# Kernel tuning notes

Hardware: AMD Instinct MI355X
Metric: run time of the kernel (lower is better)

## Reference

```python
import jax, jax.numpy as jnp
import numpy as np

B, H, W = 64, 512, 512
HW = H * W
MIN_, MAX_ = 100, 100          # seeds sampled per image (bg, fg)
MIN_P, MAX_P = 0.3, 0.3        # candidate-pool fractions
FG_ERODE_K, FG_ERODE_ITER = 11, 1
KSZ = 3                        # dilation kernel for seed maps
IGNORE_IDX = -255
N_BG = int(MIN_P * H * W)      # static bottom-n pool size
EPS = 1e-8


def _minpool2d(x, k):  # morphological erosion of binary map (geodesic border)
    return jax.lax.reduce_window(x, np.inf, jax.lax.min, (k, k), (1, 1), 'SAME')


def _maxpool3d(x, k):  # morphological dilation over (b,h,w)
    return jax.lax.reduce_window(x, -np.inf, jax.lax.max, (1, k, k), (1, 1, 1), 'SAME')


def _gumbel(u):
    return -jnp.log(-jnp.log(u))


def _one_sample(cam, u_fg, u_bg, th):
    # cam: [H,W] in [0,1]; u_fg/u_bg: [HW] uniform(0,1); th: scalar threshold
    cam_q = jnp.floor(cam * 255.0)
    th = jnp.where(th == 0.0, 1.0, jnp.where(th == 255.0, 254.0, th))
    deg = cam.min() == cam.max()  # degenerate map -> no seeds
    roi = (cam_q > th).astype(jnp.float32)
    for _ in range(FG_ERODE_ITER):
        roi = _minpool2d(roi, FG_ERODE_K)

    # ---- foreground: top-n of cam*roi, weighted sample max_ w/o replacement
    camr = (cam * roi + EPS).reshape(HW)
    n_fg = jnp.floor(MAX_P * roi.sum()).astype(jnp.int32)
    order = jnp.argsort(-camr, stable=True)                 # descending stable
    rank = jnp.zeros(HW, jnp.int32).at[order].set(jnp.arange(HW, dtype=jnp.int32))
    mask = rank < n_fg
    logp = jnp.log(jnp.where(mask, camr, 1.0))              # weighted: p = cam value
    score = jnp.where(mask, logp + _gumbel(u_fg), -jnp.inf) # Gumbel top-k == multinomial w/o repl.
    _, sel = jax.lax.top_k(score, MAX_)
    valid = (jnp.arange(MAX_) < jnp.minimum(MAX_, n_fg)) & (n_fg > 0) & (~deg)
    fg = jnp.zeros(HW, jnp.int32).at[sel].set(valid.astype(jnp.int32))

    # ---- background: bottom-n of cam, weighted by relu(1-cam)+eps
    camb = (cam + EPS).reshape(HW)
    orderb = jnp.argsort(camb, stable=True)                 # ascending stable
    rankb = jnp.zeros(HW, jnp.int32).at[orderb].set(jnp.arange(HW, dtype=jnp.int32))
    maskb = rankb < N_BG
    pb = jax.nn.relu(1.0 - camb) + EPS
    scoreb = jnp.where(maskb, jnp.log(pb) + _gumbel(u_bg), -jnp.inf)
    _, selb = jax.lax.top_k(scoreb, MIN_)
    validb = (jnp.arange(MIN_) < min(MIN_, N_BG)) & (~deg)
    bg = jnp.zeros(HW, jnp.int32).at[selb].set(validb.astype(jnp.int32))

    return fg.reshape(H, W), bg.reshape(H, W)


def setup_inputs() -> dict:
    key = jax.random.key(0)
    k1, k2, k3, k4 = jax.random.split(key, 4)
    x = jax.random.uniform(k1, (B, 1, H, W), dtype=jnp.float32)
    roi_thresh = jax.random.randint(k2, (B,), 0, 200).astype(jnp.float32)
    u_fg = jax.random.uniform(k3, (B, HW), dtype=jnp.float32, minval=1e-6, maxval=1.0)
    u_bg = jax.random.uniform(k4, (B, HW), dtype=jnp.float32, minval=1e-6, maxval=1.0)
    return {"x": x, "roi_thresh": roi_thresh, "u_fg": u_fg, "u_bg": u_bg}


def reference(x, roi_thresh, u_fg, u_bg):
    cam = x[:, 0]  # [B,H,W]
    all_fg, all_bg = jax.vmap(_one_sample)(cam, u_fg, u_bg, roi_thresh)
    if KSZ > 1:
        all_fg = (_maxpool3d(all_fg.astype(jnp.float32), KSZ) > 0.5).astype(jnp.int32)
        all_bg = (_maxpool3d(all_bg.astype(jnp.float32), KSZ) > 0.5).astype(jnp.int32)
    outer = all_fg + all_bg
    all_fg = jnp.where(outer == 2, 0, all_fg)
    all_bg = jnp.where(outer == 2, 0, all_bg)
    out = jnp.full((B, H, W), IGNORE_IDX, dtype=jnp.int32)
    out = jnp.where(all_fg == 1, 1, out)
    out = jnp.where(all_bg == 1, 0, out)
    return out
```

## Files before the change

### kernel.cpp

```cpp
#include <hip/hip_runtime.h>

typedef unsigned int u32;

#define BB 64
#define HH 512
#define WW 512
#define HWP 262144
#define WPI 8192
#define NBV 1024
#define NBS 512
#define EPSF 1e-8f
#define NBGK 78643
#define CAND_CAP 4096
#define SEL_CAP 128
#define PN 20


__device__ __forceinline__ int vbucket(float vb){
    int b = (int)(vb * (float)NBV);
    b = b < 0 ? 0 : b;
    return b > (NBV-1) ? (NBV-1) : b;
}
__device__ __forceinline__ int sbucket(float s){
    float a = (s + 24.0f) * ((float)NBS / 44.0f);
    a = fmaxf(a, 0.0f);
    int b = (int)a;
    return b > (NBS-1) ? (NBS-1) : b;
}
__device__ __forceinline__ u32 flipf(float s){
    u32 u = __float_as_uint(s);
    u32 m = (u & 0x80000000u) ? 0xFFFFFFFFu : 0x80000000u;
    return u ^ m;
}

__device__ __forceinline__ void imgblk(int bid, int& img, int& blk){
    int r = bid & 7, s = bid >> 3;
    img = ((s >> 5) << 3) | r;
    blk = s & 31;
}

__global__ __launch_bounds__(256) void k_prep(const float* __restrict__ x,
        const float* __restrict__ thr, u32* __restrict__ roiH,
        u32* __restrict__ ghist_bg, u32* __restrict__ minb, u32* __restrict__ maxb)
{
    __shared__ u32 hist[NBV];
    __shared__ u32 A[256];
    int t = threadIdx.x;
    for (int i = t; i < NBV; i += 256) hist[i] = 0u;
    A[t] = 0u;
    __syncthreads();
    int img, blk;
    imgblk(blockIdx.x, img, blk);
    const float4* c4 = (const float4*)x + (size_t)img * (HWP/4) + (size_t)blk * 2048;
    float th = thr[img];
    th = (th == 0.0f) ? 1.0f : ((th == 255.0f) ? 254.0f : th);
    u32 mn = 0xFFFFFFFFu, mx = 0u;
    #pragma unroll
    for (int k = 0; k < 8; k++){
        float4 v4 = c4[k*256 + t];
        float vv[4] = {v4.x, v4.y, v4.z, v4.w};
        u32 nib = 0u;
        #pragma unroll
        for (int c = 0; c < 4; c++){
            float v = vv[c];
            u32 ub = __float_as_uint(v);
            mn = mn < ub ? mn : ub;
            mx = mx > ub ? mx : ub;
            if (floorf(v * 255.0f) > th) nib |= (1u << c);
            atomicAdd(&hist[vbucket(v + EPSF)], 1u);
        }
        if (nib) atomicOr(&A[k*32 + (t>>3)], nib << ((t&7)*4));
    }
    for (int o = 32; o >= 1; o >>= 1){
        u32 m2 = __shfl_down(mn, o); mn = mn < m2 ? mn : m2;
        u32 m3 = __shfl_down(mx, o); mx = mx > m3 ? mx : m3;
    }
    if ((t & 63) == 0){ atomicMin(&minb[img], mn); atomicMax(&maxb[img], mx); }
    __syncthreads();
    {
        int wr = t & 15;
        u32 cur = A[t];
        u32 left  = (wr > 0)  ? A[t-1] : 0xFFFFFFFFu;
        u32 right = (wr < 15) ? A[t+1] : 0xFFFFFFFFu;
        u32 res = cur;
        #pragma unroll
        for (int d = 1; d <= 5; d++){
            res &= (cur >> d) | (right << (32 - d));
            res &= (cur << d) | (left  >> (32 - d));
        }
        roiH[(size_t)img*WPI + blk*256 + t] = res;
    }
    for (int i = t; i < NBV; i += 256){
        u32 h = hist[i];
        if (h) atomicAdd(&ghist_bg[(size_t)img*NBV + i], h);
    }
}

__global__ __launch_bounds__(256) void k_vfg(const float* __restrict__ x,
        const u32* __restrict__ roiH, u32* __restrict__ roiE,
        u32* __restrict__ roiSum, u32* __restrict__ ghist_fg)
{
    __shared__ u32 hist[NBV];
    __shared__ u32 W[256];
    int t = threadIdx.x;
    for (int i = t; i < NBV; i += 256) hist[i] = 0u;
    int img, blk;
    imgblk(blockIdx.x, img, blk);
    const u32* rp = roiH + (size_t)img * WPI;
    int iw = blk*256 + t;
    int r = iw >> 4;
    u32 res = 0xFFFFFFFFu;
    #pragma unroll
    for (int d = -5; d <= 5; d++){
        int rr = r + d;
        if (rr >= 0 && rr < HH) res &= rp[iw + d*16];
    }
    W[t] = res;
    roiE[(size_t)img*WPI + iw] = res;
    u32 cnt = __popc(res);
    for (int o = 32; o >= 1; o >>= 1) cnt += __shfl_down(cnt, o);
    if ((t & 63) == 0) atomicAdd(&roiSum[img], cnt);
    __syncthreads();
    const float4* c4 = (const float4*)x + (size_t)img * (HWP/4) + (size_t)blk * 2048;
    #pragma unroll
    for (int k = 0; k < 8; k++){
        u32 nib = (W[k*32 + (t>>3)] >> ((t&7)*4)) & 0xFu;
        if (nib){
            float4 v4 = c4[k*256 + t];
            float vv[4] = {v4.x, v4.y, v4.z, v4.w};
            #pragma unroll
            for (int c = 0; c < 4; c++){
                if ((nib >> c) & 1u) atomicAdd(&hist[vbucket(vv[c] + EPSF)], 1u);
            }
        }
    }
    __syncthreads();
    for (int i = t; i < NBV; i += 256){
        u32 h = hist[i];
        if (h) atomicAdd(&ghist_fg[(size_t)img*NBV + i], h);
    }
}

__global__ __launch_bounds__(256) void k_bound1(const u32* __restrict__ ghf, const u32* __restrict__ ghb,
        const u32* __restrict__ minb, const u32* __restrict__ maxb, const u32* __restrict__ roiSum,
        int* __restrict__ prm)
{
    int b = blockIdx.x, t = threadIdx.x;
    __shared__ int partial[256];
    __shared__ int res[2];
    int deg = (minb[b] == maxb[b]) ? 1 : 0;
    int nfg = (int)floorf(0.3f * (float)(int)roiSum[b]);
    int Bf = -1, rf = 0, Bb = -1, rb = 0;
    if (!deg && nfg > 0){
        const u32* hh = ghf + (size_t)b * NBV;
        int s = 0;
        for (int i = 0; i < 4; i++) s += (int)hh[NBV-1 - (t*4+i)];
        partial[t] = s;
        __syncthreads();
        if (t == 0){
            int cum = 0, q = 0;
            for (; q < 256; q++){ if (cum + partial[q] >= nfg) break; cum += partial[q]; }
            for (int i = 0; i < 4; i++){
                int bkt = NBV-1 - (q*4+i);
                int h = (int)hh[bkt];
                if (cum + h >= nfg){ res[0] = bkt; res[1] = nfg - cum; break; }
                cum += h;
            }
        }
        __syncthreads();
        Bf = res[0]; rf = res[1];
        __syncthreads();
    }
    if (!deg){
        const u32* hh = ghb + (size_t)b * NBV;
        int s = 0;
        for (int i = 0; i < 4; i++) s += (int)hh[t*4+i];
        partial[t] = s;
        __syncthreads();
        if (t == 0){
            int cum = 0, q = 0;
            for (; q < 256; q++){ if (cum + partial[q] >= NBGK) break; cum += partial[q]; }
            for (int i = 0; i < 4; i++){
                int bkt = q*4+i;
                int h = (int)hh[bkt];
                if (cum + h >= NBGK){ res[0] = bkt; res[1] = NBGK - cum; break; }
                cum += h;
            }
        }
        __syncthreads();
        Bb = res[0]; rb = res[1];
    }
    if (t == 0){
        int* p = prm + b * PN;
        p[0] = nfg; p[1] = deg; p[2] = Bf; p[3] = rf; p[4] = Bb; p[5] = rb;
    }
}

__global__ __launch_bounds__(256) void k_collect1(const float* __restrict__ x, const u32* __restrict__ roiE,
        const int* __restrict__ prm,
        uint2* __restrict__ candF, u32* __restrict__ cntF,
        uint2* __restrict__ candB, u32* __restrict__ cntB)
{
    __shared__ u32 words[256];
    int img, blk;
    imgblk(blockIdx.x, img, blk);
    int t = threadIdx.x;
    int Bf = prm[img*PN + 2];
    int Bb = prm[img*PN + 4];
    words[t] = roiE[(size_t)img*WPI + blk*256 + t];
    __syncthreads();
    const float4* c4 = (const float4*)x + (size_t)img * (HWP/4) + (size_t)blk * 2048;
    #pragma unroll
    for (int k = 0; k < 8; k++){
        float4 v4 = c4[k*256 + t];
        float vv[4] = {v4.x, v4.y, v4.z, v4.w};
        u32 nib = (words[k*32 + (t>>3)] >> ((t&7)*4)) & 0xFu;
        int pix0 = blk*8192 + k*1024 + t*4;
        #pragma unroll
        for (int c = 0; c < 4; c++){
            float vb = vv[c] + EPSF;
            int bkt = vbucket(vb);
            int pix = pix0 + c;
            if (bkt == Bb){
                u32 q = atomicAdd(&cntB[img], 1u);
                if (q < CAND_CAP) candB[(size_t)img*CAND_CAP + q] = make_uint2(__float_as_uint(vb), (u32)pix);
            }
            if (bkt == Bf && ((nib >> c) & 1u)){
                u32 q = atomicAdd(&cntF[img], 1u);
                if (q < CAND_CAP) candF[(size_t)img*CAND_CAP + q] = make_uint2(__float_as_uint(vb), (u32)pix);
            }
        }
    }
}

__global__ __launch_bounds__(256) void k_resolve1(const uint2* __restrict__ candF, const u32* __restrict__ cntF,
        const uint2* __restrict__ candB, const u32* __restrict__ cntB, int* __restrict__ prm)
{
    int b = blockIdx.x, t = threadIdx.x;
    __shared__ uint2 c[CAND_CAP];
    int rf = prm[b*PN + 3];
    if (rf > 0){
        int m = (int)cntF[b]; m = m < CAND_CAP ? m : CAND_CAP;
        for (int i = t; i < m; i += 256) c[i] = candF[(size_t)b*CAND_CAP + i];
        __syncthreads();
        for (int i = t; i < m; i += 256){
            u32 ki = c[i].x, xi = c[i].y;
            int r = 0;
            for (int j = 0; j < m; j++){
                u32 kj = c[j].x, xj = c[j].y;
                r += (kj > ki) || (kj == ki && xj < xi);
            }
            if (r == rf - 1){ prm[b*PN + 6] = (int)ki; prm[b*PN + 7] = (int)xi; }
        }
    } else if (t == 0){
        prm[b*PN + 6] = (int)0xFFFFFFFFu; prm[b*PN + 7] = -1;
    }
    __syncthreads();
    int rb = prm[b*PN + 5];
    if (rb > 0){
        int m = (int)cntB[b]; m = m < CAND_CAP ? m : CAND_CAP;
        for (int i = t; i < m; i += 256) c[i] = candB[(size_t)b*CAND_CAP + i];
        __syncthreads();
        for (int i = t; i < m; i += 256){
            u32 ki = c[i].x, xi = c[i].y;
            int r = 0;
            for (int j = 0; j < m; j++){
                u32 kj = c[j].x, xj = c[j].y;
                r += (kj < ki) || (kj == ki && xj < xi);
            }
            if (r == rb - 1){ prm[b*PN + 8] = (int)ki; prm[b*PN + 9] = (int)xi; }
        }
    } else if (t == 0){
        prm[b*PN + 8] = 0; prm[b*PN + 9] = -1;
    }
}

__global__ __launch_bounds__(256) void k_shist(const float* __restrict__ x, const u32* __restrict__ roiE,
        const float* __restrict__ ufg, const float* __restrict__ ubg, const int* __restrict__ prm,
        u32* __restrict__ shfG, u32* __restrict__ shbG)
{
    __shared__ u32 hf[NBS];
    __shared__ u32 hb[NBS];
    __shared__ u32 words[256];
    int t = threadIdx.x;
    for (int i = t; i < NBS; i += 256){ hf[i] = 0u; hb[i] = 0u; }
    int img, blk;
    imgblk(blockIdx.x, img, blk);
    words[t] = roiE[(size_t)img*WPI + blk*256 + t];
    __syncthreads();
    const int* p = prm + img*PN;
    u32 ubf = (u32)p[6]; int ibf = p[7];
    u32 ubb = (u32)p[8]; int ibb = p[9];
    size_t b4 = (size_t)img * (HWP/4) + (size_t)blk * 2048;
    const float4* c4 = (const float4*)x + b4;
    const float4* uf4 = (const float4*)ufg + b4;
    const float4* ub4 = (const float4*)ubg + b4;
    #pragma unroll
    for (int k = 0; k < 8; k++){
        float4 v4 = c4[k*256 + t];
        float vv[4] = {v4.x, v4.y, v4.z, v4.w};
        u32 nib = (words[k*32 + (t>>3)] >> ((t&7)*4)) & 0xFu;
        int pix0 = blk*8192 + k*1024 + t*4;
        float vbv[4]; bool fm[4], bm[4]; bool anyf = false, anyb = false;
        #pragma unroll
        for (int c = 0; c < 4; c++){
            float vb = vv[c] + EPSF;
            vbv[c] = vb;
            u32 bu = __float_as_uint(vb);
            int pix = pix0 + c;
            fm[c] = ((nib >> c) & 1u) && (bu > ubf || (bu == ubf && pix <= ibf));
            bm[c] = (bu < ubb || (bu == ubb && pix <= ibb));
            anyf |= fm[c]; anyb |= bm[c];
        }
        if (anyf){
            float4 u4 = uf4[k*256 + t];
            float uu[4] = {u4.x, u4.y, u4.z, u4.w};
            #pragma unroll
            for (int c = 0; c < 4; c++){
                if (fm[c]){
                    float s = logf(vbv[c]) - logf(-logf(uu[c]));
                    atomicAdd(&hf[sbucket(s)], 1u);
                }
            }
        }
        if (anyb){
            float4 u4 = ub4[k*256 + t];
            float uu[4] = {u4.x, u4.y, u4.z, u4.w};
            #pragma unroll
            for (int c = 0; c < 4; c++){
                if (bm[c]){
                    float pb = fmaxf(1.0f - vbv[c], 0.0f) + EPSF;
                    float s = logf(pb) - logf(-logf(uu[c]));
                    atomicAdd(&hb[sbucket(s)], 1u);
                }
            }
        }
    }
    __syncthreads();
    for (int i = t; i < NBS; i += 256){
        u32 h = hf[i]; if (h) atomicAdd(&shfG[(size_t)img*NBS + i], h);
        h = hb[i];     if (h) atomicAdd(&shbG[(size_t)img*NBS + i], h);
    }
}

__global__ __launch_bounds__(256) void k_bound2(const u32* __restrict__ shfG, const u32* __restrict__ shbG,
        int* __restrict__ prm)
{
    int b = blockIdx.x, t = threadIdx.x;
    __shared__ int partial[256];
    __shared__ int res[2];
    int* p = prm + b*PN;
    int nfg = p[0], deg = p[1];
    int kf = (deg || nfg <= 0) ? 0 : (nfg < 100 ? nfg : 100);
    int kb = deg ? 0 : 100;
    int sbf = 0x7FFFFFFF, needf = 0, sbb = 0x7FFFFFFF, needb = 0;
    if (kf > 0){
        const u32* hh = shfG + (size_t)b * NBS;
        int s = 0;
        for (int i = 0; i < 2; i++) s += (int)hh[NBS-1 - (t*2+i)];
        partial[t] = s;
        __syncthreads();
        if (t == 0){
            int cum = 0, q = 0;
            for (; q < 256; q++){ if (cum + partial[q] >= kf) break; cum += partial[q]; }
            for (int i = 0; i < 2; i++){
                int bkt = NBS-1 - (q*2+i);
                int h = (int)hh[bkt];
                if (cum + h >= kf){ res[0] = bkt; res[1] = kf - cum; break; }
                cum += h;
            }
        }
        __syncthreads();
        sbf = res[0]; needf = res[1];
        __syncthreads();
    }
    if (kb > 0){
        const u32* hh = shbG + (size_t)b * NBS;
        int s = 0;
        for (int i = 0; i < 2; i++) s += (int)hh[NBS-1 - (t*2+i)];
        partial[t] = s;
        __syncthreads();
        if (t == 0){
            int cum = 0, q = 0;
            for (; q < 256; q++){ if (cum + partial[q] >= kb) break; cum += partial[q]; }
            for (int i = 0; i < 2; i++){
                int bkt = NBS-1 - (q*2+i);
                int h = (int)hh[bkt];
                if (cum + h >= kb){ res[0] = bkt; res[1] = kb - cum; break; }
                cum += h;
            }
        }
        __syncthreads();
        sbb = res[0]; needb = res[1];
    }
    if (t == 0){
        p[10] = sbf; p[12] = needf; p[13] = sbb; p[15] = needb;
    }
}

__global__ __launch_bounds__(256) void k_collect2(const float* __restrict__ x, const u32* __restrict__ roiE,
        const float* __restrict__ ufg, const float* __restrict__ ubg, const int* __restrict__ prm,
        uint2* __restrict__ selF, u32* __restrict__ cntSelF, uint2* __restrict__ scandF, u32* __restrict__ cntScF,
        uint2* __restrict__ selB, u32* __restrict__ cntSelB, uint2* __restrict__ scandB, u32* __restrict__ cntScB)
{
    __shared__ u32 words[256];
    int img, blk;
    imgblk(blockIdx.x, img, blk);
    int t = threadIdx.x;
    words[t] = roiE[(size_t)img*WPI + blk*256 + t];
    __syncthreads();
    const int* p = prm + img*PN;
    u32 ubf = (u32)p[6]; int ibf = p[7];
    u32 ubb = (u32)p[8]; int ibb = p[9];
    int sbf = p[10], sbb = p[13];
    size_t b4 = (size_t)img * (HWP/4) + (size_t)blk * 2048;
    const float4* c4 = (const float4*)x + b4;
    const float4* uf4 = (const float4*)ufg + b4;
    const float4* ub4 = (const float4*)ubg + b4;
    #pragma unroll
    for (int k = 0; k < 8; k++){
        float4 v4 = c4[k*256 + t];
        float vv[4] = {v4.x, v4.y, v4.z, v4.w};
        u32 nib = (words[k*32 + (t>>3)] >> ((t&7)*4)) & 0xFu;
        int pix0 = blk*8192 + k*1024 + t*4;
        float vbv[4]; bool fm[4], bm[4]; bool anyf = false, anyb = false;
        #pragma unroll
        for (int c = 0; c < 4; c++){
            float vb = vv[c] + EPSF;
            vbv[c] = vb;
            u32 bu = __float_as_uint(vb);
            int pix = pix0 + c;
            fm[c] = ((nib >> c) & 1u) && (bu > ubf || (bu == ubf && pix <= ibf));
            bm[c] = (bu < ubb || (bu == ubb && pix <= ibb));
            anyf |= fm[c]; anyb |= bm[c];
        }
        if (anyf){
            float4 u4 = uf4[k*256 + t];
            float uu[4] = {u4.x, u4.y, u4.z, u4.w};
            #pragma unroll
            for (int c = 0; c < 4; c++){
                if (fm[c]){
                    float s = logf(vbv[c]) - logf(-logf(uu[c]));
                    int sb = sbucket(s);
                    if (sb > sbf){
                        u32 q = atomicAdd(&cntSelF[img], 1u);
                        if (q < SEL_CAP) selF[(size_t)img*SEL_CAP + q] = make_uint2(flipf(s), (u32)(pix0 + c));
                    } else if (sb == sbf){
                        u32 q = atomicAdd(&cntScF[img], 1u);
                        if (q < CAND_CAP) scandF[(size_t)img*CAND_CAP + q] = make_uint2(flipf(s), (u32)(pix0 + c));
                    }
                }
            }
        }
        if (anyb){
            float4 u4 = ub4[k*256 + t];
            float uu[4] = {u4.x, u4.y, u4.z, u4.w};
            #pragma unroll
            for (int c = 0; c < 4; c++){
                if (bm[c]){
                    float pb = fmaxf(1.0f - vbv[c], 0.0f) + EPSF;
                    float s = logf(pb) - logf(-logf(uu[c]));
                    int sb = sbucket(s);
                    if (sb > sbb){
                        u32 q = atomicAdd(&cntSelB[img], 1u);
                        if (q < SEL_CAP) selB[(size_t)img*SEL_CAP + q] = make_uint2(flipf(s), (u32)(pix0 + c));
                    } else if (sb == sbb){
                        u32 q = atomicAdd(&cntScB[img], 1u);
                        if (q < CAND_CAP) scandB[(size_t)img*CAND_CAP + q] = make_uint2(flipf(s), (u32)(pix0 + c));
                    }
                }
            }
        }
    }
}

__global__ __launch_bounds__(256) void k_seeds(
        const uint2* __restrict__ selF, const u32* __restrict__ cntSelF,
        const uint2* __restrict__ scandF, const u32* __restrict__ cntScF,
        const uint2* __restrict__ selB, const u32* __restrict__ cntSelB,
        const uint2* __restrict__ scandB, const u32* __restrict__ cntScB,
        const int* __restrict__ prm,
        int* __restrict__ gSeedF, int* __restrict__ gnF,
        int* __restrict__ gSeedB, int* __restrict__ gnB)
{
    int b = blockIdx.x, t = threadIdx.x;
    __shared__ uint2 c[CAND_CAP];
    __shared__ int seedF[SEL_CAP];
    __shared__ int seedB[SEL_CAP];
    __shared__ int nF, nB;
    const int* p = prm + b*PN;
    int needf = p[12], needb = p[15];

    int c0 = (int)cntSelF[b]; c0 = c0 < SEL_CAP ? c0 : SEL_CAP;
    for (int i = t; i < c0; i += 256) seedF[i] = (int)selF[(size_t)b*SEL_CAP + i].y;
    int m = (int)cntScF[b]; m = m < CAND_CAP ? m : CAND_CAP;
    for (int i = t; i < m; i += 256) c[i] = scandF[(size_t)b*CAND_CAP + i];
    if (t == 0){ nF = c0; nB = 0; }
    __syncthreads();
    for (int i = t; i < m; i += 256){
        u32 ki = c[i].x, xi = c[i].y;
        int r = 0;
        for (int j = 0; j < m; j++){
            u32 kj = c[j].x, xj = c[j].y;
            r += (kj > ki) || (kj == ki && xj < xi);
        }
        if (r < needf){
            int q = atomicAdd(&nF, 1);
            if (q < SEL_CAP) seedF[q] = (int)xi;
        }
    }
    __syncthreads();
    int fN = nF; fN = fN < SEL_CAP ? fN : SEL_CAP;
    __syncthreads();

    int c0b = (int)cntSelB[b]; c0b = c0b < SEL_CAP ? c0b : SEL_CAP;
    for (int i = t; i < c0b; i += 256) seedB[i] = (int)selB[(size_t)b*SEL_CAP + i].y;
    int mb = (int)cntScB[b]; mb = mb < CAND_CAP ? mb : CAND_CAP;
    for (int i = t; i < mb; i += 256) c[i] = scandB[(size_t)b*CAND_CAP + i];
    if (t == 0) nB = c0b;
    __syncthreads();
    for (int i = t; i < mb; i += 256){
        u32 ki = c[i].x, xi = c[i].y;
        int r = 0;
        for (int j = 0; j < mb; j++){
            u32 kj = c[j].x, xj = c[j].y;
            r += (kj > ki) || (kj == ki && xj < xi);
        }
        if (r < needb){
            int q = atomicAdd(&nB, 1);
            if (q < SEL_CAP) seedB[q] = (int)xi;
        }
    }
    __syncthreads();
    int bN = nB; bN = bN < SEL_CAP ? bN : SEL_CAP;

    for (int i = t; i < fN; i += 256) gSeedF[b*SEL_CAP + i] = seedF[i];
    for (int i = t; i < bN; i += 256) gSeedB[b*SEL_CAP + i] = seedB[i];
    if (t == 0){ gnF[b] = fN; gnB[b] = bN; }
}

__global__ __launch_bounds__(256) void k_paint(
        const int* __restrict__ gSeedF, const int* __restrict__ gnF,
        const int* __restrict__ gSeedB, const int* __restrict__ gnB,
        int* __restrict__ out)
{
    __shared__ int sF[SEL_CAP], sB[SEL_CAP];
    int img = blockIdx.x >> 5, blk = blockIdx.x & 31, t = threadIdx.x;
    int fN = gnF[img]; fN = fN < SEL_CAP ? fN : SEL_CAP;
    int bN = gnB[img]; bN = bN < SEL_CAP ? bN : SEL_CAP;
    for (int i = t; i < fN; i += 256) sF[i] = gSeedF[img*SEL_CAP + i];
    for (int i = t; i < bN; i += 256) sB[i] = gSeedB[img*SEL_CAP + i];
    int4* o4 = (int4*)(out + (size_t)img*HWP + blk*8192);
    for (int i = t; i < 2048; i += 256) o4[i] = make_int4(-255,-255,-255,-255);
    __syncthreads();
    int row0 = blk * 16;
    int* outp = out + (size_t)img*HWP;
    for (int task = t; task < fN * 9; task += 256){
        int s = sF[task / 9];
        int o = task % 9;
        int y = (s >> 9) + (o / 3) - 1;
        int xx = (s & 511) + (o % 3) - 1;
        if (y < row0 || y >= row0 + 16 || xx < 0 || xx >= WW) continue;
        bool conf = false;
        for (int j = 0; j < bN; j++){
            int sb2 = sB[j];
            int dy = y - (sb2 >> 9); if (dy < 0) dy = -dy;
            int dx = xx - (sb2 & 511); if (dx < 0) dx = -dx;
            if (dy <= 1 && dx <= 1){ conf = true; break; }
        }
        if (!conf) outp[y * WW + xx] = 1;
    }
    for (int task = t; task < bN * 9; task += 256){
        int s = sB[task / 9];
        int o = task % 9;
        int y = (s >> 9) + (o / 3) - 1;
        int xx = (s & 511) + (o % 3) - 1;
        if (y < row0 || y >= row0 + 16 || xx < 0 || xx >= WW) continue;
        bool conf = false;
        for (int j = 0; j < fN; j++){
            int sf2 = sF[j];
            int dy = y - (sf2 >> 9); if (dy < 0) dy = -dy;
            int dx = xx - (sf2 & 511); if (dx < 0) dx = -dx;
            if (dy <= 1 && dx <= 1){ conf = true; break; }
        }
        if (!conf) outp[y * WW + xx] = 0;
    }
}

extern "C" void kernel_launch(void* const* d_in, const int* in_sizes, int n_in,
                              void* d_out, int out_size, void* d_ws, size_t ws_size,
                              hipStream_t stream)
{
    (void)in_sizes; (void)n_in; (void)out_size; (void)ws_size;
    const float* x   = (const float*)d_in[0];
    const float* thr = (const float*)d_in[1];
    const float* ufg = (const float*)d_in[2];
    const float* ubg = (const float*)d_in[3];
    int* out = (int*)d_out;
    char* ws = (char*)d_ws;

    size_t off = 0;
    auto carve = [&](size_t bytes) -> char* {
        char* ptr = ws + off;
        off = (off + bytes + 255) & ~(size_t)255;
        return ptr;
    };
    u32* ghist_bg = (u32*)carve((size_t)BB*NBV*4);
    u32* ghist_fg = (u32*)carve((size_t)BB*NBV*4);
    u32* shf      = (u32*)carve((size_t)BB*NBS*4);
    u32* shb      = (u32*)carve((size_t)BB*NBS*4);
    u32* cnts     = (u32*)carve((size_t)6*BB*4);
    u32* roiSum   = (u32*)carve((size_t)BB*4);
    u32* maxb     = (u32*)carve((size_t)BB*4);
    size_t zero_bytes = off;
    u32* minb     = (u32*)carve((size_t)BB*4);
    size_t minb_off = (size_t)((char*)minb - ws);
    u32* roiH     = (u32*)carve((size_t)BB*WPI*4);
    u32* roiE     = (u32*)carve((size_t)BB*WPI*4);
    int* prm      = (int*)carve((size_t)BB*PN*4);
    uint2* candF  = (uint2*)carve((size_t)BB*CAND_CAP*8);
    uint2* candB  = (uint2*)carve((size_t)BB*CAND_CAP*8);
    uint2* scandF = (uint2*)carve((size_t)BB*CAND_CAP*8);
    uint2* scandB = (uint2*)carve((size_t)BB*CAND_CAP*8);
    uint2* selF   = (uint2*)carve((size_t)BB*SEL_CAP*8);
    uint2* selB   = (uint2*)carve((size_t)BB*SEL_CAP*8);
    int* gSeedF   = (int*)carve((size_t)BB*SEL_CAP*4);
    int* gSeedB   = (int*)carve((size_t)BB*SEL_CAP*4);
    int* gnF      = (int*)carve((size_t)BB*4);
    int* gnB      = (int*)carve((size_t)BB*4);
    u32* cntF = cnts, *cntB = cnts + BB, *cntSelF = cnts + 2*BB,
       *cntScF = cnts + 3*BB, *cntSelB = cnts + 4*BB, *cntScB = cnts + 5*BB;

    hipMemsetAsync(ws, 0, zero_bytes, stream);
    hipMemsetAsync(ws + minb_off, 0xFF, (size_t)BB*4, stream);

    k_prep    <<<2048, 256, 0, stream>>>(x, thr, roiH, ghist_bg, minb, maxb);
    k_vfg     <<<2048, 256, 0, stream>>>(x, roiH, roiE, roiSum, ghist_fg);
    k_bound1  <<<64,   256, 0, stream>>>(ghist_fg, ghist_bg, minb, maxb, roiSum, prm);
    k_collect1<<<2048, 256, 0, stream>>>(x, roiE, prm, candF, cntF, candB, cntB);
    k_resolve1<<<64,   256, 0, stream>>>(candF, cntF, candB, cntB, prm);
    k_shist   <<<2048, 256, 0, stream>>>(x, roiE, ufg, ubg, prm, shf, shb);
    k_bound2  <<<64,   256, 0, stream>>>(shf, shb, prm);
    k_collect2<<<2048, 256, 0, stream>>>(x, roiE, ufg, ubg, prm,
                                         selF, cntSelF, scandF, cntScF,
                                         selB, cntSelB, scandB, cntScB);
    k_seeds   <<<64,   256, 0, stream>>>(selF, cntSelF, scandF, cntScF,
                                         selB, cntSelB, scandB, cntScB, prm,
                                         gSeedF, gnF, gSeedB, gnB);
    k_paint   <<<2048, 256, 0, stream>>>(gSeedF, gnF, gSeedB, gnB, out);
}
```

Measured before the change: 517.0 us.

## Fold histogram bound kernels into collect passes, pad counters, batch loads

```diff
diff --git a/kernel.cpp b/kernel.cpp
--- a/kernel.cpp
+++ b/kernel.cpp
@@ -13,7 +13,8 @@
 #define NBGK 78643
 #define CAND_CAP 4096
 #define SEL_CAP 128
-#define PN 20
+#define PN 12
+#define CP 16
 
 
 __device__ __forceinline__ int vbucket(float vb){
@@ -33,10 +34,37 @@
     return u ^ m;
 }
 
-__device__ __forceinline__ void imgblk(int bid, int& img, int& blk){
-    int r = bid & 7, s = bid >> 3;
-    img = ((s >> 5) << 3) | r;
-    blk = s & 31;
+template<int NB, int BPT, bool DESC>
+__device__ __forceinline__ void hist_kth(const u32* __restrict__ hh, int target,
+        int* partial, int* res, int t){
+    int s = 0;
+    #pragma unroll
+    for (int i = 0; i < BPT; i++){
+        int b = DESC ? (NB-1 - (t*BPT+i)) : (t*BPT+i);
+        s += (int)hh[b];
+    }
+    partial[t] = s;
+    __syncthreads();
+    for (int off = 1; off < 256; off <<= 1){
+        int v = partial[t];
+        int u = (t >= off) ? partial[t-off] : 0;
+        __syncthreads();
+        partial[t] = v + u;
+        __syncthreads();
+    }
+    int incl = partial[t];
+    int above = incl - s;
+    if (above < target && target <= incl){
+        int cum = above;
+        #pragma unroll
+        for (int i = 0; i < BPT; i++){
+            int b = DESC ? (NB-1 - (t*BPT+i)) : (t*BPT+i);
+            int h = (int)hh[b];
+            if (cum + h >= target){ res[0] = b; res[1] = target - cum; break; }
+            cum += h;
+        }
+    }
+    __syncthreads();
 }
 
 __global__ __launch_bounds__(256) void k_prep(const float* __restrict__ x,
@@ -49,25 +77,26 @@
     for (int i = t; i < NBV; i += 256) hist[i] = 0u;
     A[t] = 0u;
     __syncthreads();
-    int img, blk;
-    imgblk(blockIdx.x, img, blk);
+    int img = blockIdx.x >> 5, blk = blockIdx.x & 31;
     const float4* c4 = (const float4*)x + (size_t)img * (HWP/4) + (size_t)blk * 2048;
     float th = thr[img];
     th = (th == 0.0f) ? 1.0f : ((th == 255.0f) ? 254.0f : th);
+    float4 v[8];
+    #pragma unroll
+    for (int k = 0; k < 8; k++) v[k] = c4[k*256 + t];
     u32 mn = 0xFFFFFFFFu, mx = 0u;
     #pragma unroll
     for (int k = 0; k < 8; k++){
-        float4 v4 = c4[k*256 + t];
-        float vv[4] = {v4.x, v4.y, v4.z, v4.w};
+        float vv[4] = {v[k].x, v[k].y, v[k].z, v[k].w};
         u32 nib = 0u;
         #pragma unroll
         for (int c = 0; c < 4; c++){
-            float v = vv[c];
-            u32 ub = __float_as_uint(v);
+            float vl = vv[c];
+            u32 ub = __float_as_uint(vl);
             mn = mn < ub ? mn : ub;
             mx = mx > ub ? mx : ub;
-            if (floorf(v * 255.0f) > th) nib |= (1u << c);
-            atomicAdd(&hist[vbucket(v + EPSF)], 1u);
+            if (floorf(vl * 255.0f) > th) nib |= (1u << c);
+            atomicAdd(&hist[vbucket(vl + EPSF)], 1u);
         }
         if (nib) atomicOr(&A[k*32 + (t>>3)], nib << ((t&7)*4));
     }
@@ -104,8 +133,7 @@
     __shared__ u32 W[256];
     int t = threadIdx.x;
     for (int i = t; i < NBV; i += 256) hist[i] = 0u;
-    int img, blk;
-    imgblk(blockIdx.x, img, blk);
+    int img = blockIdx.x >> 5, blk = blockIdx.x & 31;
     const u32* rp = roiH + (size_t)img * WPI;
     int iw = blk*256 + t;
     int r = iw >> 4;
@@ -122,15 +150,20 @@
     if ((t & 63) == 0) atomicAdd(&roiSum[img], cnt);
     __syncthreads();
     const float4* c4 = (const float4*)x + (size_t)img * (HWP/4) + (size_t)blk * 2048;
-    #pragma unroll
-    for (int k = 0; k < 8; k++){
-        u32 nib = (W[k*32 + (t>>3)] >> ((t&7)*4)) & 0xFu;
-        if (nib){
-            float4 v4 = c4[k*256 + t];
-            float vv[4] = {v4.x, v4.y, v4.z, v4.w};
+    u32 nb[8];
+    float4 vv[8];
+    #pragma unroll
+    for (int k = 0; k < 8; k++){
+        nb[k] = (W[k*32 + (t>>3)] >> ((t&7)*4)) & 0xFu;
+        if (nb[k]) vv[k] = c4[k*256 + t];
+    }
+    #pragma unroll
+    for (int k = 0; k < 8; k++){
+        if (nb[k]){
+            float vl[4] = {vv[k].x, vv[k].y, vv[k].z, vv[k].w};
             #pragma unroll
             for (int c = 0; c < 4; c++){
-                if ((nib >> c) & 1u) atomicAdd(&hist[vbucket(vv[c] + EPSF)], 1u);
+                if ((nb[k] >> c) & 1u) atomicAdd(&hist[vbucket(vl[c] + EPSF)], 1u);
             }
         }
     }
@@ -141,79 +174,41 @@
     }
 }
 
-__global__ __launch_bounds__(256) void k_bound1(const u32* __restrict__ ghf, const u32* __restrict__ ghb,
+__global__ __launch_bounds__(256) void k_collect1(const float* __restrict__ x, const u32* __restrict__ roiE,
+        const u32* __restrict__ ghf, const u32* __restrict__ ghb,
         const u32* __restrict__ minb, const u32* __restrict__ maxb, const u32* __restrict__ roiSum,
-        int* __restrict__ prm)
-{
-    int b = blockIdx.x, t = threadIdx.x;
+        int* __restrict__ prm,
+        uint2* __restrict__ candF, u32* __restrict__ cntF,
+        uint2* __restrict__ candB, u32* __restrict__ cntB)
+{
     __shared__ int partial[256];
     __shared__ int res[2];
-    int deg = (minb[b] == maxb[b]) ? 1 : 0;
-    int nfg = (int)floorf(0.3f * (float)(int)roiSum[b]);
+    __shared__ u32 words[256];
+    int img = blockIdx.x >> 5, blk = blockIdx.x & 31, t = threadIdx.x;
+    int deg = (minb[img] == maxb[img]) ? 1 : 0;
+    int nfg = (int)floorf(0.3f * (float)(int)roiSum[img]);
     int Bf = -1, rf = 0, Bb = -1, rb = 0;
     if (!deg && nfg > 0){
-        const u32* hh = ghf + (size_t)b * NBV;
-        int s = 0;
-        for (int i = 0; i < 4; i++) s += (int)hh[NBV-1 - (t*4+i)];
-        partial[t] = s;
-        __syncthreads();
-        if (t == 0){
-            int cum = 0, q = 0;
-            for (; q < 256; q++){ if (cum + partial[q] >= nfg) break; cum += partial[q]; }
-            for (int i = 0; i < 4; i++){
-                int bkt = NBV-1 - (q*4+i);
-                int h = (int)hh[bkt];
-                if (cum + h >= nfg){ res[0] = bkt; res[1] = nfg - cum; break; }
-                cum += h;
-            }
-        }
-        __syncthreads();
+        hist_kth<NBV,4,true>(ghf + (size_t)img*NBV, nfg, partial, res, t);
         Bf = res[0]; rf = res[1];
-        __syncthreads();
     }
     if (!deg){
-        const u32* hh = ghb + (size_t)b * NBV;
-        int s = 0;
-        for (int i = 0; i < 4; i++) s += (int)hh[t*4+i];
-        partial[t] = s;
-        __syncthreads();
-        if (t == 0){
-            int cum = 0, q = 0;
-            for (; q < 256; q++){ if (cum + partial[q] >= NBGK) break; cum += partial[q]; }
-            for (int i = 0; i < 4; i++){
-                int bkt = q*4+i;
-                int h = (int)hh[bkt];
-                if (cum + h >= NBGK){ res[0] = bkt; res[1] = NBGK - cum; break; }
-                cum += h;
-            }
-        }
-        __syncthreads();
+        hist_kth<NBV,4,false>(ghb + (size_t)img*NBV, NBGK, partial, res, t);
         Bb = res[0]; rb = res[1];
     }
-    if (t == 0){
-        int* p = prm + b * PN;
+    if (blk == 0 && t == 0){
+        int* p = prm + img*PN;
         p[0] = nfg; p[1] = deg; p[2] = Bf; p[3] = rf; p[4] = Bb; p[5] = rb;
     }
-}
-
-__global__ __launch_bounds__(256) void k_collect1(const float* __restrict__ x, const u32* __restrict__ roiE,
-        const int* __restrict__ prm,
-        uint2* __restrict__ candF, u32* __restrict__ cntF,
-        uint2* __restrict__ candB, u32* __restrict__ cntB)
-{
-    __shared__ u32 words[256];
-    int img, blk;
-    imgblk(blockIdx.x, img, blk);
-    int t = threadIdx.x;
-    int Bf = prm[img*PN + 2];
-    int Bb = prm[img*PN + 4];
     words[t] = roiE[(size_t)img*WPI + blk*256 + t];
     __syncthreads();
     const float4* c4 = (const float4*)x + (size_t)img * (HWP/4) + (size_t)blk * 2048;
-    #pragma unroll
-    for (int k = 0; k < 8; k++){
-        float4 v4 = c4[k*256 + t];
-        float vv[4] = {v4.x, v4.y, v4.z, v4.w};
+    float4 v[8];
+    #pragma unroll
+    for (int k = 0; k < 8; k++) v[k] = c4[k*256 + t];
+    #pragma unroll
+    for (int k = 0; k < 8; k++){
+        float vv[4] = {v[k].x, v[k].y, v[k].z, v[k].w};
         u32 nib = (words[k*32 + (t>>3)] >> ((t&7)*4)) & 0xFu;
         int pix0 = blk*8192 + k*1024 + t*4;
         #pragma unroll
@@ -222,11 +217,11 @@
             int bkt = vbucket(vb);
             int pix = pix0 + c;
             if (bkt == Bb){
-                u32 q = atomicAdd(&cntB[img], 1u);
+                u32 q = atomicAdd(&cntB[img*CP], 1u);
                 if (q < CAND_CAP) candB[(size_t)img*CAND_CAP + q] = make_uint2(__float_as_uint(vb), (u32)pix);
             }
             if (bkt == Bf && ((nib >> c) & 1u)){
-                u32 q = atomicAdd(&cntF[img], 1u);
+                u32 q = atomicAdd(&cntF[img*CP], 1u);
                 if (q < CAND_CAP) candF[(size_t)img*CAND_CAP + q] = make_uint2(__float_as_uint(vb), (u32)pix);
             }
         }
@@ -240,7 +235,7 @@
     __shared__ uint2 c[CAND_CAP];
     int rf = prm[b*PN + 3];
     if (rf > 0){
-        int m = (int)cntF[b]; m = m < CAND_CAP ? m : CAND_CAP;
+        int m = (int)cntF[b*CP]; m = m < CAND_CAP ? m : CAND_CAP;
         for (int i = t; i < m; i += 256) c[i] = candF[(size_t)b*CAND_CAP + i];
         __syncthreads();
         for (int i = t; i < m; i += 256){
@@ -258,7 +253,7 @@
     __syncthreads();
     int rb = prm[b*PN + 5];
     if (rb > 0){
-        int m = (int)cntB[b]; m = m < CAND_CAP ? m : CAND_CAP;
+        int m = (int)cntB[b*CP]; m = m < CAND_CAP ? m : CAND_CAP;
         for (int i = t; i < m; i += 256) c[i] = candB[(size_t)b*CAND_CAP + i];
         __syncthreads();
         for (int i = t; i < m; i += 256){
@@ -284,8 +279,7 @@
     __shared__ u32 words[256];
     int t = threadIdx.x;
     for (int i = t; i < NBS; i += 256){ hf[i] = 0u; hb[i] = 0u; }
-    int img, blk;
-    imgblk(blockIdx.x, img, blk);
+    int img = blockIdx.x >> 5, blk = blockIdx.x & 31;
     words[t] = roiE[(size_t)img*WPI + blk*256 + t];
     __syncthreads();
     const int* p = prm + img*PN;
@@ -295,41 +289,53 @@
     const float4* c4 = (const float4*)x + b4;
     const float4* uf4 = (const float4*)ufg + b4;
     const float4* ub4 = (const float4*)ubg + b4;
-    #pragma unroll
-    for (int k = 0; k < 8; k++){
-        float4 v4 = c4[k*256 + t];
-        float vv[4] = {v4.x, v4.y, v4.z, v4.w};
+    float4 v[8];
+    #pragma unroll
+    for (int k = 0; k < 8; k++) v[k] = c4[k*256 + t];
+    u32 fmsk = 0u, bmsk = 0u;
+    #pragma unroll
+    for (int k = 0; k < 8; k++){
+        float vv[4] = {v[k].x, v[k].y, v[k].z, v[k].w};
         u32 nib = (words[k*32 + (t>>3)] >> ((t&7)*4)) & 0xFu;
         int pix0 = blk*8192 + k*1024 + t*4;
-        float vbv[4]; bool fm[4], bm[4]; bool anyf = false, anyb = false;
         #pragma unroll
         for (int c = 0; c < 4; c++){
             float vb = vv[c] + EPSF;
-            vbv[c] = vb;
             u32 bu = __float_as_uint(vb);
             int pix = pix0 + c;
-            fm[c] = ((nib >> c) & 1u) && (bu > ubf || (bu == ubf && pix <= ibf));
-            bm[c] = (bu < ubb || (bu == ubb && pix <= ibb));
-            anyf |= fm[c]; anyb |= bm[c];
-        }
-        if (anyf){
-            float4 u4 = uf4[k*256 + t];
-            float uu[4] = {u4.x, u4.y, u4.z, u4.w};
+            if (((nib >> c) & 1u) && (bu > ubf || (bu == ubf && pix <= ibf))) fmsk |= 1u << (k*4+c);
+            if (bu < ubb || (bu == ubb && pix <= ibb)) bmsk |= 1u << (k*4+c);
+        }
+    }
+    float4 uf[8];
+    #pragma unroll
+    for (int k = 0; k < 8; k++) if ((fmsk >> (k*4)) & 0xFu) uf[k] = uf4[k*256 + t];
+    #pragma unroll
+    for (int k = 0; k < 8; k++){
+        if ((fmsk >> (k*4)) & 0xFu){
+            float vv[4] = {v[k].x, v[k].y, v[k].z, v[k].w};
+            float uu[4] = {uf[k].x, uf[k].y, uf[k].z, uf[k].w};
             #pragma unroll
             for (int c = 0; c < 4; c++){
-                if (fm[c]){
-                    float s = logf(vbv[c]) - logf(-logf(uu[c]));
+                if ((fmsk >> (k*4+c)) & 1u){
+                    float s = logf(vv[c] + EPSF) - logf(-logf(uu[c]));
                     atomicAdd(&hf[sbucket(s)], 1u);
                 }
             }
         }
-        if (anyb){
-            float4 u4 = ub4[k*256 + t];
-            float uu[4] = {u4.x, u4.y, u4.z, u4.w};
+    }
+    float4 ub[8];
+    #pragma unroll
+    for (int k = 0; k < 8; k++) if ((bmsk >> (k*4)) & 0xFu) ub[k] = ub4[k*256 + t];
+    #pragma unroll
+    for (int k = 0; k < 8; k++){
+        if ((bmsk >> (k*4)) & 0xFu){
+            float vv[4] = {v[k].x, v[k].y, v[k].z, v[k].w};
+            float uu[4] = {ub[k].x, ub[k].y, ub[k].z, ub[k].w};
             #pragma unroll
             for (int c = 0; c < 4; c++){
-                if (bm[c]){
-                    float pb = fmaxf(1.0f - vbv[c], 0.0f) + EPSF;
+                if ((bmsk >> (k*4+c)) & 1u){
+                    float pb = fmaxf(1.0f - (vv[c] + EPSF), 0.0f) + EPSF;
                     float s = logf(pb) - logf(-logf(uu[c]));
                     atomicAdd(&hb[sbucket(s)], 1u);
                 }
@@ -343,129 +349,100 @@
     }
 }
 
-__global__ __launch_bounds__(256) void k_bound2(const u32* __restrict__ shfG, const u32* __restrict__ shbG,
-        int* __restrict__ prm)
-{
-    int b = blockIdx.x, t = threadIdx.x;
+__global__ __launch_bounds__(256) void k_collect2(const float* __restrict__ x, const u32* __restrict__ roiE,
+        const float* __restrict__ ufg, const float* __restrict__ ubg, const int* __restrict__ prm,
+        const u32* __restrict__ shfG, const u32* __restrict__ shbG,
+        uint2* __restrict__ selF, u32* __restrict__ cntSelF, uint2* __restrict__ scandF, u32* __restrict__ cntScF,
+        uint2* __restrict__ selB, u32* __restrict__ cntSelB, uint2* __restrict__ scandB, u32* __restrict__ cntScB)
+{
     __shared__ int partial[256];
     __shared__ int res[2];
-    int* p = prm + b*PN;
+    __shared__ u32 words[256];
+    int img = blockIdx.x >> 5, blk = blockIdx.x & 31, t = threadIdx.x;
+    const int* p = prm + img*PN;
     int nfg = p[0], deg = p[1];
     int kf = (deg || nfg <= 0) ? 0 : (nfg < 100 ? nfg : 100);
     int kb = deg ? 0 : 100;
-    int sbf = 0x7FFFFFFF, needf = 0, sbb = 0x7FFFFFFF, needb = 0;
+    int sbf = 0x7FFFFFFF, sbb = 0x7FFFFFFF;
     if (kf > 0){
-        const u32* hh = shfG + (size_t)b * NBS;
-        int s = 0;
-        for (int i = 0; i < 2; i++) s += (int)hh[NBS-1 - (t*2+i)];
-        partial[t] = s;
-        __syncthreads();
-        if (t == 0){
-            int cum = 0, q = 0;
-            for (; q < 256; q++){ if (cum + partial[q] >= kf) break; cum += partial[q]; }
-            for (int i = 0; i < 2; i++){
-                int bkt = NBS-1 - (q*2+i);
-                int h = (int)hh[bkt];
-                if (cum + h >= kf){ res[0] = bkt; res[1] = kf - cum; break; }
-                cum += h;
-            }
-        }
-        __syncthreads();
-        sbf = res[0]; needf = res[1];
-        __syncthreads();
+        hist_kth<NBS,2,true>(shfG + (size_t)img*NBS, kf, partial, res, t);
+        sbf = res[0];
     }
     if (kb > 0){
-        const u32* hh = shbG + (size_t)b * NBS;
-        int s = 0;
-        for (int i = 0; i < 2; i++) s += (int)hh[NBS-1 - (t*2+i)];
-        partial[t] = s;
-        __syncthreads();
-        if (t == 0){
-            int cum = 0, q = 0;
-            for (; q < 256; q++){ if (cum + partial[q] >= kb) break; cum += partial[q]; }
-            for (int i = 0; i < 2; i++){
-                int bkt = NBS-1 - (q*2+i);
-                int h = (int)hh[bkt];
-                if (cum + h >= kb){ res[0] = bkt; res[1] = kb - cum; break; }
-                cum += h;
-            }
-        }
-        __syncthreads();
-        sbb = res[0]; needb = res[1];
-    }
-    if (t == 0){
-        p[10] = sbf; p[12] = needf; p[13] = sbb; p[15] = needb;
-    }
-}
-
-__global__ __launch_bounds__(256) void k_collect2(const float* __restrict__ x, const u32* __restrict__ roiE,
-        const float* __restrict__ ufg, const float* __restrict__ ubg, const int* __restrict__ prm,
-        uint2* __restrict__ selF, u32* __restrict__ cntSelF, uint2* __restrict__ scandF, u32* __restrict__ cntScF,
-        uint2* __restrict__ selB, u32* __restrict__ cntSelB, uint2* __restrict__ scandB, u32* __restrict__ cntScB)
-{
-    __shared__ u32 words[256];
-    int img, blk;
-    imgblk(blockIdx.x, img, blk);
-    int t = threadIdx.x;
-    words[t] = roiE[(size_t)img*WPI + blk*256 + t];
-    __syncthreads();
-    const int* p = prm + img*PN;
+        hist_kth<NBS,2,true>(shbG + (size_t)img*NBS, kb, partial, res, t);
+        sbb = res[0];
+    }
     u32 ubf = (u32)p[6]; int ibf = p[7];
     u32 ubb = (u32)p[8]; int ibb = p[9];
-    int sbf = p[10], sbb = p[13];
+    words[t] = roiE[(size_t)img*WPI + blk*256 + t];
+    __syncthreads();
     size_t b4 = (size_t)img * (HWP/4) + (size_t)blk * 2048;
     const float4* c4 = (const float4*)x + b4;
     const float4* uf4 = (const float4*)ufg + b4;
     const float4* ub4 = (const float4*)ubg + b4;
-    #pragma unroll
-    for (int k = 0; k < 8; k++){
-        float4 v4 = c4[k*256 + t];
-        float vv[4] = {v4.x, v4.y, v4.z, v4.w};
+    float4 v[8];
+    #pragma unroll
+    for (int k = 0; k < 8; k++) v[k] = c4[k*256 + t];
+    u32 fmsk = 0u, bmsk = 0u;
+    #pragma unroll
+    for (int k = 0; k < 8; k++){
+        float vv[4] = {v[k].x, v[k].y, v[k].z, v[k].w};
         u32 nib = (words[k*32 + (t>>3)] >> ((t&7)*4)) & 0xFu;
         int pix0 = blk*8192 + k*1024 + t*4;
-        float vbv[4]; bool fm[4], bm[4]; bool anyf = false, anyb = false;
         #pragma unroll
         for (int c = 0; c < 4; c++){
             float vb = vv[c] + EPSF;
-            vbv[c] = vb;
             u32 bu = __float_as_uint(vb);
             int pix = pix0 + c;
-            fm[c] = ((nib >> c) & 1u) && (bu > ubf || (bu == ubf && pix <= ibf));
-            bm[c] = (bu < ubb || (bu == ubb && pix <= ibb));
-            anyf |= fm[c]; anyb |= bm[c];
-        }
-        if (anyf){
-            float4 u4 = uf4[k*256 + t];
-            float uu[4] = {u4.x, u4.y, u4.z, u4.w};
+            if (((nib >> c) & 1u) && (bu > ubf || (bu == ubf && pix <= ibf))) fmsk |= 1u << (k*4+c);
+            if (bu < ubb || (bu == ubb && pix <= ibb)) bmsk |= 1u << (k*4+c);
+        }
+    }
+    float4 uf[8];
+    #pragma unroll
+    for (int k = 0; k < 8; k++) if ((fmsk >> (k*4)) & 0xFu) uf[k] = uf4[k*256 + t];
+    #pragma unroll
+    for (int k = 0; k < 8; k++){
+        if ((fmsk >> (k*4)) & 0xFu){
+            float vv[4] = {v[k].x, v[k].y, v[k].z, v[k].w};
+            float uu[4] = {uf[k].x, uf[k].y, uf[k].z, uf[k].w};
+            int pix0 = blk*8192 + k*1024 + t*4;
             #pragma unroll
             for (int c = 0; c < 4; c++){
-                if (fm[c]){
-                    float s = logf(vbv[c]) - logf(-logf(uu[c]));
+                if ((fmsk >> (k*4+c)) & 1u){
+                    float s = logf(vv[c] + EPSF) - logf(-logf(uu[c]));
                     int sb = sbucket(s);
                     if (sb > sbf){
-                        u32 q = atomicAdd(&cntSelF[img], 1u);
+                        u32 q = atomicAdd(&cntSelF[img*CP], 1u);
                         if (q < SEL_CAP) selF[(size_t)img*SEL_CAP + q] = make_uint2(flipf(s), (u32)(pix0 + c));
                     } else if (sb == sbf){
-                        u32 q = atomicAdd(&cntScF[img], 1u);
+                        u32 q = atomicAdd(&cntScF[img*CP], 1u);
                         if (q < CAND_CAP) scandF[(size_t)img*CAND_CAP + q] = make_uint2(flipf(s), (u32)(pix0 + c));
                     }
                 }
             }
         }
-        if (anyb){
-            float4 u4 = ub4[k*256 + t];
-            float uu[4] = {u4.x, u4.y, u4.z, u4.w};
+    }
+    float4 ub[8];
+    #pragma unroll
+    for (int k = 0; k < 8; k++) if ((bmsk >> (k*4)) & 0xFu) ub[k] = ub4[k*256 + t];
+    #pragma unroll
+    for (int k = 0; k < 8; k++){
+        if ((bmsk >> (k*4)) & 0xFu){
+            float vv[4] = {v[k].x, v[k].y, v[k].z, v[k].w};
+            float uu[4] = {ub[k].x, ub[k].y, ub[k].z, ub[k].w};
+            int pix0 = blk*8192 + k*1024 + t*4;
             #pragma unroll
             for (int c = 0; c < 4; c++){
-                if (bm[c]){
-                    float pb = fmaxf(1.0f - vbv[c], 0.0f) + EPSF;
+                if ((bmsk >> (k*4+c)) & 1u){
+                    float pb = fmaxf(1.0f - (vv[c] + EPSF), 0.0f) + EPSF;
                     float s = logf(pb) - logf(-logf(uu[c]));
                     int sb = sbucket(s);
                     if (sb > sbb){
-                        u32 q = atomicAdd(&cntSelB[img], 1u);
+                        u32 q = atomicAdd(&cntSelB[img*CP], 1u);
                         if (q < SEL_CAP) selB[(size_t)img*SEL_CAP + q] = make_uint2(flipf(s), (u32)(pix0 + c));
                     } else if (sb == sbb){
-                        u32 q = atomicAdd(&cntScB[img], 1u);
+                        u32 q = atomicAdd(&cntScB[img*CP], 1u);
                         if (q < CAND_CAP) scandB[(size_t)img*CAND_CAP + q] = make_uint2(flipf(s), (u32)(pix0 + c));
                     }
                 }
@@ -479,21 +456,35 @@
         const uint2* __restrict__ scandF, const u32* __restrict__ cntScF,
         const uint2* __restrict__ selB, const u32* __restrict__ cntSelB,
         const uint2* __restrict__ scandB, const u32* __restrict__ cntScB,
+        const u32* __restrict__ shfG, const u32* __restrict__ shbG,
         const int* __restrict__ prm,
         int* __restrict__ gSeedF, int* __restrict__ gnF,
         int* __restrict__ gSeedB, int* __restrict__ gnB)
 {
     int b = blockIdx.x, t = threadIdx.x;
     __shared__ uint2 c[CAND_CAP];
+    __shared__ int partial[256];
+    __shared__ int res[2];
     __shared__ int seedF[SEL_CAP];
     __shared__ int seedB[SEL_CAP];
     __shared__ int nF, nB;
     const int* p = prm + b*PN;
-    int needf = p[12], needb = p[15];
-
-    int c0 = (int)cntSelF[b]; c0 = c0 < SEL_CAP ? c0 : SEL_CAP;
+    int nfg = p[0], deg = p[1];
+    int kf = (deg || nfg <= 0) ? 0 : (nfg < 100 ? nfg : 100);
+    int kb = deg ? 0 : 100;
+    int needf = 0, needb = 0;
+    if (kf > 0){
+        hist_kth<NBS,2,true>(shfG + (size_t)b*NBS, kf, partial, res, t);
+        needf = res[1];
+    }
+    if (kb > 0){
+        hist_kth<NBS,2,true>(shbG + (size_t)b*NBS, kb, partial, res, t);
+        needb = res[1];
+    }
+
+    int c0 = (int)cntSelF[b*CP]; c0 = c0 < SEL_CAP ? c0 : SEL_CAP;
     for (int i = t; i < c0; i += 256) seedF[i] = (int)selF[(size_t)b*SEL_CAP + i].y;
-    int m = (int)cntScF[b]; m = m < CAND_CAP ? m : CAND_CAP;
+    int m = (int)cntScF[b*CP]; m = m < CAND_CAP ? m : CAND_CAP;
     for (int i = t; i < m; i += 256) c[i] = scandF[(size_t)b*CAND_CAP + i];
     if (t == 0){ nF = c0; nB = 0; }
     __syncthreads();
@@ -513,9 +504,9 @@
     int fN = nF; fN = fN < SEL_CAP ? fN : SEL_CAP;
     __syncthreads();
 
-    int c0b = (int)cntSelB[b]; c0b = c0b < SEL_CAP ? c0b : SEL_CAP;
+    int c0b = (int)cntSelB[b*CP]; c0b = c0b < SEL_CAP ? c0b : SEL_CAP;
     for (int i = t; i < c0b; i += 256) seedB[i] = (int)selB[(size_t)b*SEL_CAP + i].y;
-    int mb = (int)cntScB[b]; mb = mb < CAND_CAP ? mb : CAND_CAP;
+    int mb = (int)cntScB[b*CP]; mb = mb < CAND_CAP ? mb : CAND_CAP;
     for (int i = t; i < mb; i += 256) c[i] = scandB[(size_t)b*CAND_CAP + i];
     if (t == 0) nB = c0b;
     __syncthreads();
@@ -551,7 +542,8 @@
     for (int i = t; i < fN; i += 256) sF[i] = gSeedF[img*SEL_CAP + i];
     for (int i = t; i < bN; i += 256) sB[i] = gSeedB[img*SEL_CAP + i];
     int4* o4 = (int4*)(out + (size_t)img*HWP + blk*8192);
-    for (int i = t; i < 2048; i += 256) o4[i] = make_int4(-255,-255,-255,-255);
+    #pragma unroll
+    for (int i = 0; i < 8; i++) o4[i*256 + t] = make_int4(-255,-255,-255,-255);
     __syncthreads();
     int row0 = blk * 16;
     int* outp = out + (size_t)img*HWP;
@@ -609,7 +601,7 @@
     u32* ghist_fg = (u32*)carve((size_t)BB*NBV*4);
     u32* shf      = (u32*)carve((size_t)BB*NBS*4);
     u32* shb      = (u32*)carve((size_t)BB*NBS*4);
-    u32* cnts     = (u32*)carve((size_t)6*BB*4);
+    u32* cnts     = (u32*)carve((size_t)6*BB*CP*4);
     u32* roiSum   = (u32*)carve((size_t)BB*4);
     u32* maxb     = (u32*)carve((size_t)BB*4);
     size_t zero_bytes = off;
@@ -628,24 +620,23 @@
     int* gSeedB   = (int*)carve((size_t)BB*SEL_CAP*4);
     int* gnF      = (int*)carve((size_t)BB*4);
     int* gnB      = (int*)carve((size_t)BB*4);
-    u32* cntF = cnts, *cntB = cnts + BB, *cntSelF = cnts + 2*BB,
-       *cntScF = cnts + 3*BB, *cntSelB = cnts + 4*BB, *cntScB = cnts + 5*BB;
+    u32* cntF = cnts, *cntB = cnts + BB*CP, *cntSelF = cnts + 2*BB*CP,
+       *cntScF = cnts + 3*BB*CP, *cntSelB = cnts + 4*BB*CP, *cntScB = cnts + 5*BB*CP;
 
     hipMemsetAsync(ws, 0, zero_bytes, stream);
     hipMemsetAsync(ws + minb_off, 0xFF, (size_t)BB*4, stream);
 
     k_prep    <<<2048, 256, 0, stream>>>(x, thr, roiH, ghist_bg, minb, maxb);
     k_vfg     <<<2048, 256, 0, stream>>>(x, roiH, roiE, roiSum, ghist_fg);
-    k_bound1  <<<64,   256, 0, stream>>>(ghist_fg, ghist_bg, minb, maxb, roiSum, prm);
-    k_collect1<<<2048, 256, 0, stream>>>(x, roiE, prm, candF, cntF, candB, cntB);
+    k_collect1<<<2048, 256, 0, stream>>>(x, roiE, ghist_fg, ghist_bg, minb, maxb, roiSum,
+                                         prm, candF, cntF, candB, cntB);
     k_resolve1<<<64,   256, 0, stream>>>(candF, cntF, candB, cntB, prm);
     k_shist   <<<2048, 256, 0, stream>>>(x, roiE, ufg, ubg, prm, shf, shb);
-    k_bound2  <<<64,   256, 0, stream>>>(shf, shb, prm);
-    k_collect2<<<2048, 256, 0, stream>>>(x, roiE, ufg, ubg, prm,
+    k_collect2<<<2048, 256, 0, stream>>>(x, roiE, ufg, ubg, prm, shf, shb,
                                          selF, cntSelF, scandF, cntScF,
                                          selB, cntSelB, scandB, cntScB);
     k_seeds   <<<64,   256, 0, stream>>>(selF, cntSelF, scandF, cntScF,
-                                         selB, cntSelB, scandB, cntScB, prm,
-                                         gSeedF, gnF, gSeedB, gnB);
+                                         selB, cntSelB, scandB, cntScB,
+                                         shf, shb, prm, gSeedF, gnF, gSeedB, gnB);
     k_paint   <<<2048, 256, 0, stream>>>(gSeedF, gnF, gSeedB, gnB, out);
 }
```

New measurement: 451.1 us. 1.15x faster.
